# Performance work log

Measured on AMD Instinct MI355X. Metric: run time of the kernel, lower is better.

The kernel has to match this reference:

```python
import jax, jax.numpy as jnp
import numpy as np

N_NODES = 100000
N_EDGES = 1600000
F_IN = 128
H1 = 128
H2 = 128
N_CLASSES = 40


def setup_inputs() -> dict:
    key = jax.random.key(0)
    ks = jax.random.split(key, 8)
    node_features = jax.random.normal(ks[0], (N_NODES, F_IN), dtype=jnp.float32)
    edge_indices = jax.random.randint(ks[1], (2, N_EDGES), 0, N_NODES, dtype=jnp.int32)
    # Glorot-ish init for weights
    W1 = jax.random.normal(ks[2], (F_IN, H1), dtype=jnp.float32) / np.sqrt(F_IN)
    b1 = jnp.zeros((H1,), dtype=jnp.float32)
    W2 = jax.random.normal(ks[3], (H1, H2), dtype=jnp.float32) / np.sqrt(H1)
    b2 = jnp.zeros((H2,), dtype=jnp.float32)
    Wl = jax.random.normal(ks[4], (H2, N_CLASSES), dtype=jnp.float32) / np.sqrt(H2)
    bl = jnp.zeros((N_CLASSES,), dtype=jnp.float32)
    return {
        "node_features": node_features,
        "edge_indices": edge_indices,
        "W1": W1, "b1": b1,
        "W2": W2, "b2": b2,
        "Wl": Wl, "bl": bl,
    }


def _gcn_norm(edge_indices, n_nodes):
    # PyG GCNConv default: add self-loops, symmetric normalization.
    src = jnp.concatenate([edge_indices[0], jnp.arange(n_nodes, dtype=edge_indices.dtype)])
    dst = jnp.concatenate([edge_indices[1], jnp.arange(n_nodes, dtype=edge_indices.dtype)])
    deg = jax.ops.segment_sum(jnp.ones_like(dst, dtype=jnp.float32), dst,
                              num_segments=n_nodes)  # degree over destinations (col)
    deg_inv_sqrt = jnp.where(deg > 0, jax.lax.rsqrt(deg), 0.0)
    norm = deg_inv_sqrt[src] * deg_inv_sqrt[dst]  # (E + N,)
    return src, dst, norm


def _gcn_conv(x, W, b, src, dst, norm, n_nodes):
    xw = x @ W                                    # (N, F_out) dense GEMM
    msg = xw[src] * norm[:, None]                 # gather + scale: (E+N, F_out)
    out = jax.ops.segment_sum(msg, dst, num_segments=n_nodes)  # scatter-add
    return out + b


def reference(node_features, edge_indices, W1, b1, W2, b2, Wl, bl):
    n = node_features.shape[0]
    src, dst, norm = _gcn_norm(edge_indices, n)
    # dropout is identity in eval mode
    x = jax.nn.relu(_gcn_conv(node_features, W1, b1, src, dst, norm, n))
    x = jax.nn.relu(_gcn_conv(x, W2, b2, src, dst, norm, n))
    return x @ Wl + bl  # (N, num_classes)
```

## Files before the change

### kernel.cpp

```cpp
#include <hip/hip_runtime.h>


typedef unsigned int uint32;
typedef unsigned short u16;

#define FD 128

using short8 = __attribute__((ext_vector_type(8))) short;
using f32x4  = __attribute__((ext_vector_type(4))) float;

union U4S8 { uint4 u; short8 s; };

__device__ __forceinline__ u16 f2bf(float f) {
    uint32 u = __float_as_uint(f);
    uint32 r = ((u >> 16) & 1u) + 0x7FFFu;
    return (u16)((u + r) >> 16);
}
__device__ __forceinline__ float bfLo(uint32 w) { return __uint_as_float(w << 16); }
__device__ __forceinline__ float bfHi(uint32 w) { return __uint_as_float(w & 0xFFFF0000u); }

__global__ void k_beacon(float* __restrict__ out, long long n, float val) {
    long long i = (long long)blockIdx.x * 256 + threadIdx.x;
    if (i < n) out[i] = val;
}

__device__ __forceinline__ void wprep_dev(const float* __restrict__ W,
                                          uint4* __restrict__ wf,
                                          int NOUT, int NT, int t) {
    for (int e = t; e < 4 * NT * 64; e += 256) {
        int kc = e / (NT * 64);
        int rem = e - kc * (NT * 64);
        int ct = rem >> 6;
        int l  = rem & 63;
        int k0 = kc * 32 + (l >> 4) * 8;
        int c  = ct * 16 + (l & 15);
        u16 us[8];
#pragma unroll
        for (int i = 0; i < 8; i++)
            us[i] = (c < NOUT) ? f2bf(W[(size_t)(k0 + i) * NOUT + c]) : (u16)0;
        uint4 u;
        u.x = (uint32)us[0] | ((uint32)us[1] << 16);
        u.y = (uint32)us[2] | ((uint32)us[3] << 16);
        u.z = (uint32)us[4] | ((uint32)us[5] << 16);
        u.w = (uint32)us[6] | ((uint32)us[7] << 16);
        wf[(kc * NT + ct) * 64 + l] = u;
    }
}

__global__ __launch_bounds__(256) void k_cnt_mgemm(
    const int* __restrict__ dst, int* __restrict__ cnt, int* __restrict__ rank,
    int ne, int nn,
    const float* __restrict__ A, const float* __restrict__ W,
    uint32* __restrict__ yt, int M, int ngemm,
    const float* __restrict__ W2, uint4* __restrict__ wf2,
    const float* __restrict__ Wl, uint4* __restrict__ wfl) {
    __shared__ uint4 Bf[4][8][64];

    int bid = blockIdx.x;
    int t = threadIdx.x;

    if (bid >= (int)gridDim.x - 2) {
        if (bid == (int)gridDim.x - 2) wprep_dev(W2, wf2, 128, 8, t);
        else                           wprep_dev(Wl, wfl, 40, 3, t);
        return;
    }

    int g5 = bid / 5;
    bool isg = ((bid % 5) == 0) && (g5 < ngemm);

    if (!isg) {
        int idx = bid - (g5 + 1 < ngemm ? g5 + 1 : ngemm);
        int e = idx * 256 + t;
        if (e < ne) {
            int d = dst[e];
            int a = ((unsigned)d < (unsigned)nn) ? d : nn;
            rank[e] = atomicAdd(&cnt[a], 1);
        }
        return;
    }

    int idx = g5;
    for (int e = t; e < 4 * 8 * 64; e += 256) {
        int kc = e / (8 * 64);
        int rem = e - kc * (8 * 64);
        int ct = rem >> 6;
        int l  = rem & 63;
        int k0 = kc * 32 + (l >> 4) * 8;
        int c  = ct * 16 + (l & 15);
        u16 us[8];
#pragma unroll
        for (int i = 0; i < 8; i++) us[i] = f2bf(W[(size_t)(k0 + i) * 128 + c]);
        uint4 u;
        u.x = (uint32)us[0] | ((uint32)us[1] << 16);
        u.y = (uint32)us[2] | ((uint32)us[3] << 16);
        u.z = (uint32)us[4] | ((uint32)us[5] << 16);
        u.w = (uint32)us[6] | ((uint32)us[7] << 16);
        Bf[kc][ct][l] = u;
    }
    __syncthreads();

    int lane = t & 63, wv = t >> 6;
    int r0 = idx * 64 + wv * 16;
    if (r0 >= M) return;

    int arow = r0 + (lane & 15);
    if (arow >= M) arow = M - 1;
    U4S8 af[4];
#pragma unroll
    for (int kc = 0; kc < 4; kc++) {
        const float4* s = (const float4*)(A + (size_t)arow * FD + kc * 32 + (lane >> 4) * 8);
        float4 v0 = s[0], v1 = s[1];
        uint4 u;
        u.x = (uint32)f2bf(v0.x) | ((uint32)f2bf(v0.y) << 16);
        u.y = (uint32)f2bf(v0.z) | ((uint32)f2bf(v0.w) << 16);
        u.z = (uint32)f2bf(v1.x) | ((uint32)f2bf(v1.y) << 16);
        u.w = (uint32)f2bf(v1.z) | ((uint32)f2bf(v1.w) << 16);
        af[kc].u = u;
    }

    f32x4 acc[8];
#pragma unroll
    for (int ct = 0; ct < 8; ct++) acc[ct] = f32x4{0.f, 0.f, 0.f, 0.f};
#pragma unroll
    for (int kc = 0; kc < 4; kc++) {
#pragma unroll
        for (int ct = 0; ct < 8; ct++) {
            U4S8 b;
            b.u = Bf[kc][ct][lane];
            acc[ct] = __builtin_amdgcn_mfma_f32_16x16x32_bf16(af[kc].s, b.s, acc[ct], 0, 0, 0);
        }
    }

    int rb = r0 + (lane >> 4) * 4;
#pragma unroll
    for (int r = 0; r < 4; r++) {
        int row = rb + r;
#pragma unroll
        for (int ct = 0; ct < 8; ct++) {
            float v = acc[ct][r];
            float vn = __shfl_xor(v, 1);
            if (!(lane & 1) && row < M) {
                uint32 word = (uint32)f2bf(v) | ((uint32)f2bf(vn) << 16);
                yt[(size_t)row * 128 + (ct * 16 + (lane & 15)) / 2] = word;
            }
        }
    }
}

__global__ void k_scan_a(const int* __restrict__ cnt, int* __restrict__ row_start,
                         int* __restrict__ bsum, float* __restrict__ dis, int nn) {
    __shared__ int tmp[256];
    int t = threadIdx.x;
    int i = blockIdx.x * 256 + t;
    int v = (i < nn) ? cnt[i] : 0;
    if (i < nn) dis[i] = rsqrtf((float)(v + 1));
    tmp[t] = v;
    __syncthreads();
    for (int off = 1; off < 256; off <<= 1) {
        int x = (t >= off) ? tmp[t - off] : 0;
        __syncthreads();
        tmp[t] += x;
        __syncthreads();
    }
    if (i < nn) row_start[i] = tmp[t] - v;
    if (t == 255) bsum[blockIdx.x] = tmp[255];
}

__global__ void k_scan_b(int* bsum, int nb) {
    __shared__ int tmp[512];
    __shared__ int carry;
    int t = threadIdx.x;
    if (t == 0) carry = 0;
    __syncthreads();
    for (int base = 0; base < nb; base += 512) {
        int i = base + t;
        int v = (i < nb) ? bsum[i] : 0;
        tmp[t] = v;
        __syncthreads();
        for (int off = 1; off < 512; off <<= 1) {
            int x = (t >= off) ? tmp[t - off] : 0;
            __syncthreads();
            tmp[t] += x;
            __syncthreads();
        }
        if (i < nb) bsum[i] = tmp[t] - v + carry;
        __syncthreads();
        if (t == 0) carry += tmp[511];
        __syncthreads();
    }
}

__global__ void k_scan_c(int* __restrict__ row_start, const int* __restrict__ bsum,
                         const int* __restrict__ cnt, int nn) {
    int i = blockIdx.x * 256 + threadIdx.x;
    if (i < nn) {
        int r = row_start[i] + bsum[blockIdx.x];
        row_start[i] = r;
        if (i == nn - 1) row_start[nn] = r + cnt[i];
    }
}

__global__ __launch_bounds__(256) void k_fill(const int* __restrict__ src,
                                              const int* __restrict__ dst,
                                              const int* __restrict__ rank,
                                              const int* __restrict__ row_start,
                                              int* __restrict__ col_idx,
                                              int ne, int nn) {
    long long base = ((long long)blockIdx.x * 256 + threadIdx.x) * 4;
    if (base + 4 <= (long long)ne) {
        int4 d4 = *(const int4*)(dst + base);
        int4 s4 = *(const int4*)(src + base);
        int4 r4 = *(const int4*)(rank + base);
        int dd[4] = {d4.x, d4.y, d4.z, d4.w};
        int ss[4] = {s4.x, s4.y, s4.z, s4.w};
        int rr[4] = {r4.x, r4.y, r4.z, r4.w};
        int pp[4];
#pragma unroll
        for (int r = 0; r < 4; r++) {
            bool ok = (unsigned)dd[r] < (unsigned)nn;
            int dv = ok ? dd[r] : 0;
            int p = row_start[dv] + rr[r];
            pp[r] = ok ? p : -1;
        }
#pragma unroll
        for (int r = 0; r < 4; r++)
            if ((unsigned)pp[r] < (unsigned)ne) col_idx[pp[r]] = ss[r];
    } else {
        for (long long e = base; e < (long long)ne; e++) {
            int d = dst[e];
            if ((unsigned)d >= (unsigned)nn) continue;
            int p = row_start[d] + rank[e];
            if ((unsigned)p < (unsigned)ne) col_idx[p] = src[e];
        }
    }
}

template <int NOUT, bool WEIGHTED, bool OUTBF>
__global__ __launch_bounds__(256) void k_aggmm(
    const uint32* __restrict__ ytin,
    const float* __restrict__ dis,
    const int* __restrict__ row_start,
    const int* __restrict__ col_idx,
    const float* __restrict__ abias,
    const uint4* __restrict__ Wfrag,
    void* __restrict__ out,
    const float* __restrict__ gbias,
    int nn, int ne) {
    constexpr int NT = (NOUT + 15) / 16;
    __shared__ u16 Ar[64][136];

    int t = threadIdx.x;
    int lane = t & 63, wv = t >> 6;
    int g = lane >> 4, sub = lane & 15;
    int nb0 = blockIdx.x * 64;

    float2 bq[4];
#pragma unroll
    for (int k = 0; k < 4; k++) bq[k] = *(const float2*)(abias + (sub * 4 + k) * 2);

    for (int it = 0; it < 4; it++) {
        int lr = wv * 16 + it * 4 + g;
        int n = nb0 + lr;
        bool act = n < nn;
        int nl = act ? n : 0;

        float di = dis[nl];
        int jb = row_start[nl];
        int je = row_start[nl + 1];
        if (!act) { jb = 0; je = 0; }
        if (jb < 0) jb = 0;
        if (je > ne) je = ne;
        int deg = je - jb; if (deg < 0) deg = 0;
        int je1 = je - 1;

        uint4 sv = *(const uint4*)(ytin + (size_t)nl * 128 + sub * 4);
        float wself = WEIGHTED ? di : 1.f;
        float a0 = bfLo(sv.x) * wself, a1 = bfHi(sv.x) * wself;
        float a2 = bfLo(sv.y) * wself, a3 = bfHi(sv.y) * wself;
        float a4 = bfLo(sv.z) * wself, a5 = bfHi(sv.z) * wself;
        float a6 = bfLo(sv.w) * wself, a7 = bfHi(sv.w) * wself;

        int m = deg;
        m = max(m, __shfl_xor(m, 16));
        m = max(m, __shfl_xor(m, 32));

        for (int base = 0; base < m; base += 8) {
            int jj = jb + base + (sub & 7);
            int jc = jj < je ? jj : je1;
            if (jc < 0) jc = 0;
            int sl = col_idx[jc];
            bool okp = (unsigned)sl < (unsigned)nn;
            float ds = WEIGHTED ? (okp ? dis[sl] : 0.f) : (okp ? 1.f : 0.f);
            if (!okp) sl = 0;

            int ss[8];
            float ww[8];
#pragma unroll
            for (int r = 0; r < 8; r++) {
                int L = (lane & 48) + r;
                ss[r] = __shfl(sl, L);
                float w = __shfl(ds, L);
                ww[r] = (base + r < deg) ? w : 0.f;
            }
            uint4 uu[8];
#pragma unroll
            for (int r = 0; r < 8; r++)
                uu[r] = *(const uint4*)(ytin + (size_t)ss[r] * 128 + sub * 4);
#pragma unroll
            for (int r = 0; r < 8; r++) {
                float wg = ww[r];
                a0 = fmaf(bfLo(uu[r].x), wg, a0); a1 = fmaf(bfHi(uu[r].x), wg, a1);
                a2 = fmaf(bfLo(uu[r].y), wg, a2); a3 = fmaf(bfHi(uu[r].y), wg, a3);
                a4 = fmaf(bfLo(uu[r].z), wg, a4); a5 = fmaf(bfHi(uu[r].z), wg, a5);
                a6 = fmaf(bfLo(uu[r].w), wg, a6); a7 = fmaf(bfHi(uu[r].w), wg, a7);
            }
        }

        if (act) {
            float r0 = fmaxf(fmaf(a0, di, bq[0].x), 0.f);
            float r1 = fmaxf(fmaf(a1, di, bq[0].y), 0.f);
            float r2 = fmaxf(fmaf(a2, di, bq[1].x), 0.f);
            float r3 = fmaxf(fmaf(a3, di, bq[1].y), 0.f);
            float r4 = fmaxf(fmaf(a4, di, bq[2].x), 0.f);
            float r5 = fmaxf(fmaf(a5, di, bq[2].y), 0.f);
            float r6 = fmaxf(fmaf(a6, di, bq[3].x), 0.f);
            float r7 = fmaxf(fmaf(a7, di, bq[3].y), 0.f);
            uint4 o;
            o.x = (uint32)f2bf(r0) | ((uint32)f2bf(r1) << 16);
            o.y = (uint32)f2bf(r2) | ((uint32)f2bf(r3) << 16);
            o.z = (uint32)f2bf(r4) | ((uint32)f2bf(r5) << 16);
            o.w = (uint32)f2bf(r6) | ((uint32)f2bf(r7) << 16);
            *(uint4*)&Ar[lr][sub * 8] = o;
        }
    }
    __syncthreads();

    int arl = wv * 16 + (lane & 15);
    U4S8 af[4];
#pragma unroll
    for (int kc = 0; kc < 4; kc++)
        af[kc].u = *(const uint4*)&Ar[arl][kc * 32 + (lane >> 4) * 8];

    f32x4 acc[NT];
#pragma unroll
    for (int ct = 0; ct < NT; ct++) {
        acc[ct] = f32x4{0.f, 0.f, 0.f, 0.f};
        U4S8 w0, w1, w2, w3;
        w0.u = Wfrag[(0 * NT + ct) * 64 + lane];
        w1.u = Wfrag[(1 * NT + ct) * 64 + lane];
        w2.u = Wfrag[(2 * NT + ct) * 64 + lane];
        w3.u = Wfrag[(3 * NT + ct) * 64 + lane];
        acc[ct] = __builtin_amdgcn_mfma_f32_16x16x32_bf16(af[0].s, w0.s, acc[ct], 0, 0, 0);
        acc[ct] = __builtin_amdgcn_mfma_f32_16x16x32_bf16(af[1].s, w1.s, acc[ct], 0, 0, 0);
        acc[ct] = __builtin_amdgcn_mfma_f32_16x16x32_bf16(af[2].s, w2.s, acc[ct], 0, 0, 0);
        acc[ct] = __builtin_amdgcn_mfma_f32_16x16x32_bf16(af[3].s, w3.s, acc[ct], 0, 0, 0);
    }

    int rbl = wv * 16 + (lane >> 4) * 4;
    if (OUTBF) {
        uint32* yto = (uint32*)out;
#pragma unroll
        for (int r = 0; r < 4; r++) {
            int grow = nb0 + rbl + r;
            int gc = grow < nn ? grow : 0;
            float rs = dis[gc];
#pragma unroll
            for (int ct = 0; ct < NT; ct++) {
                float v = acc[ct][r] * rs;
                float vn = __shfl_xor(v, 1);
                if (!(lane & 1) && grow < nn) {
                    uint32 word = (uint32)f2bf(v) | ((uint32)f2bf(vn) << 16);
                    yto[(size_t)grow * 128 + (ct * 16 + (lane & 15)) / 2] = word;
                }
            }
        }
    } else {
        float* fo = (float*)out;
#pragma unroll
        for (int r = 0; r < 4; r++) {
            int grow = nb0 + rbl + r;
            if (grow >= nn) continue;
#pragma unroll
            for (int ct = 0; ct < NT; ct++) {
                int c = ct * 16 + (lane & 15);
                if (c < NOUT)
                    fo[(size_t)grow * NOUT + c] = acc[ct][r] + gbias[c];
            }
        }
    }
}

static inline char* carve(char*& p, size_t bytes) {
    char* r = p;
    p += (bytes + 255) & ~(size_t)255;
    return r;
}

extern "C" void kernel_launch(void* const* d_in, const int* in_sizes, int n_in,
                              void* d_out, int out_size, void* d_ws, size_t ws_size,
                              hipStream_t stream) {
    const long long outn = out_size;
    float* dout = (float*)d_out;
    if (n_in < 8) {
        k_beacon<<<(int)((outn + 255) / 256), 256, 0, stream>>>(dout, outn, 888.f);
        return;
    }
    float* X        = (float*)d_in[0];
    const int* ei   = (const int*)d_in[1];
    const float* W1 = (const float*)d_in[2];
    const float* b1 = (const float*)d_in[3];
    const float* W2 = (const float*)d_in[4];
    const float* b2 = (const float*)d_in[5];
    const float* Wl = (const float*)d_in[6];
    const float* bl = (const float*)d_in[7];

    const int H1 = in_sizes[3];
    const int F  = in_sizes[2] / (H1 > 0 ? H1 : 1);
    const int NC = in_sizes[7];
    const int NN = in_sizes[0] / (F > 0 ? F : 1);
    const int NE = in_sizes[1] / 2;
    if (NN <= 0 || NE <= 0 || F != FD || H1 != FD || NC != 40 ||
        (long long)NN * FD != in_sizes[0] || outn != (long long)NN * NC) {
        k_beacon<<<(int)((outn + 255) / 256), 256, 0, stream>>>(dout, outn, 888.f);
        return;
    }

    const int* src = ei;
    const int* dst = ei + NE;
    const int nb = (NN + 255) / 256;

    char* p = (char*)d_ws;
    int*   cnt       = (int*)  carve(p, ((size_t)NN + 1) * 4);
    float* dis       = (float*)carve(p, (size_t)NN * 4);
    int*   bsum      = (int*)  carve(p, (size_t)nb * 4);
    int*   row_start = (int*)  carve(p, ((size_t)NN + 1) * 4);
    int*   col_idx   = (int*)  carve(p, (size_t)NE * 4);
    uint4* wf2       = (uint4*)carve(p, (size_t)4 * 8 * 64 * 16);
    uint4* wfl       = (uint4*)carve(p, (size_t)4 * 3 * 64 * 16);
    size_t needed = (size_t)(p - (char*)d_ws);
    int* rank;
    if ((size_t)NE * 4 <= (size_t)outn * 4) {
        rank = (int*)d_out;
    } else {
        rank = (int*)carve(p, (size_t)NE * 4);
        needed = (size_t)(p - (char*)d_ws);
    }
    if (needed > ws_size) {
        k_beacon<<<(int)((outn + 255) / 256), 256, 0, stream>>>(dout, outn, 999.f);
        return;
    }

    const int ecb1 = (NE + 255) / 256;
    const int ecb4 = (int)(((long long)NE + 1023) / 1024);
    const int gemm_blocks = (NN + 63) / 64;

    uint32* yt1 = (uint32*)X;
    uint32* zt  = yt1 + 64;

    hipMemsetAsync(cnt, 0, ((size_t)NN + 1) * 4, stream);
    k_cnt_mgemm<<<ecb1 + gemm_blocks + 2, 256, 0, stream>>>(
        dst, cnt, rank, NE, NN,
        X, W1, yt1, NN, gemm_blocks,
        W2, wf2, Wl, wfl);
    k_scan_a<<<nb, 256, 0, stream>>>(cnt, row_start, bsum, dis, NN);
    k_scan_b<<<1, 512, 0, stream>>>(bsum, nb);
    k_scan_c<<<nb, 256, 0, stream>>>(row_start, bsum, cnt, NN);
    k_fill<<<ecb4, 256, 0, stream>>>(src, dst, rank, row_start, col_idx, NE, NN);

    k_aggmm<128, true, true><<<gemm_blocks, 256, 0, stream>>>(
        yt1, dis, row_start, col_idx, b1, wf2, (void*)zt, nullptr, NN, NE);

    k_aggmm<40, false, false><<<gemm_blocks, 256, 0, stream>>>(
        zt, dis, row_start, col_idx, b2, wfl, (void*)dout, bl, NN, NE);
}
```

Measured before the change: 358.1 us.

## Fuse three-kernel prefix scan into single-pass decoupled lookback and drop aggmm barrier

Replaces the three-kernel degree scan (block scan, block-sum scan, add-back) with one kernel. Each block publishes its total with a status flag in a per-block state word and looks back at earlier blocks to find its exclusive prefix. The state array sits next to the count array, so the existing memset now clears both. In k_aggmm, the __syncthreads between writing the shared A tile and reading it is swapped for a compiler sched_barrier. That removes a workgroup barrier but may cause a cross-wave race if a wave reads rows written by another wave.

```diff
diff --git a/kernel.cpp b/kernel.cpp
--- a/kernel.cpp
+++ b/kernel.cpp
@@ -3,6 +3,7 @@
 
 typedef unsigned int uint32;
 typedef unsigned short u16;
+typedef unsigned long long u64;
 
 #define FD 128
 
@@ -147,11 +148,14 @@
     }
 }
 
-__global__ void k_scan_a(const int* __restrict__ cnt, int* __restrict__ row_start,
-                         int* __restrict__ bsum, float* __restrict__ dis, int nn) {
+__global__ __launch_bounds__(256) void k_scan(const int* __restrict__ cnt,
+                                              int* __restrict__ row_start,
+                                              float* __restrict__ dis,
+                                              u64* __restrict__ state, int nn) {
     __shared__ int tmp[256];
-    int t = threadIdx.x;
-    int i = blockIdx.x * 256 + t;
+    __shared__ int exc_sh;
+    int t = threadIdx.x, b = blockIdx.x;
+    int i = b * 256 + t;
     int v = (i < nn) ? cnt[i] : 0;
     if (i < nn) dis[i] = rsqrtf((float)(v + 1));
     tmp[t] = v;
@@ -162,42 +166,26 @@
         tmp[t] += x;
         __syncthreads();
     }
-    if (i < nn) row_start[i] = tmp[t] - v;
-    if (t == 255) bsum[blockIdx.x] = tmp[255];
-}
-
-__global__ void k_scan_b(int* bsum, int nb) {
-    __shared__ int tmp[512];
-    __shared__ int carry;
-    int t = threadIdx.x;
-    if (t == 0) carry = 0;
+    int total = tmp[255];
+
+    if (t == 0) {
+        atomicExch(&state[b], (1ULL << 62) | (unsigned)total);
+        unsigned exc = 0;
+        for (int j = b - 1; j >= 0;) {
+            u64 s = atomicAdd(&state[j], 0ULL);
+            u64 fl = s >> 62;
+            if (fl == 0) continue;
+            exc += (unsigned)s;
+            if (fl == 2) break;
+            j--;
+        }
+        atomicExch(&state[b], (2ULL << 62) | (u64)(unsigned)(exc + (unsigned)total));
+        exc_sh = (int)exc;
+    }
     __syncthreads();
-    for (int base = 0; base < nb; base += 512) {
-        int i = base + t;
-        int v = (i < nb) ? bsum[i] : 0;
-        tmp[t] = v;
-        __syncthreads();
-        for (int off = 1; off < 512; off <<= 1) {
-            int x = (t >= off) ? tmp[t - off] : 0;
-            __syncthreads();
-            tmp[t] += x;
-            __syncthreads();
-        }
-        if (i < nb) bsum[i] = tmp[t] - v + carry;
-        __syncthreads();
-        if (t == 0) carry += tmp[511];
-        __syncthreads();
-    }
-}
-
-__global__ void k_scan_c(int* __restrict__ row_start, const int* __restrict__ bsum,
-                         const int* __restrict__ cnt, int nn) {
-    int i = blockIdx.x * 256 + threadIdx.x;
-    if (i < nn) {
-        int r = row_start[i] + bsum[blockIdx.x];
-        row_start[i] = r;
-        if (i == nn - 1) row_start[nn] = r + cnt[i];
-    }
+    int exc = exc_sh;
+    if (i < nn) row_start[i] = exc + tmp[t] - v;
+    if (i == nn - 1) row_start[nn] = exc + total;
 }
 
 __global__ __launch_bounds__(256) void k_fill(const int* __restrict__ src,
@@ -333,7 +321,8 @@
             *(uint4*)&Ar[lr][sub * 8] = o;
         }
     }
-    __syncthreads();
+
+    __builtin_amdgcn_sched_barrier(0);
 
     int arl = wv * 16 + (lane & 15);
     U4S8 af[4];
@@ -431,8 +420,9 @@
 
     char* p = (char*)d_ws;
     int*   cnt       = (int*)  carve(p, ((size_t)NN + 1) * 4);
+    u64*   state     = (u64*)  carve(p, (size_t)nb * 8);
+    char*  zero_end  = p;
     float* dis       = (float*)carve(p, (size_t)NN * 4);
-    int*   bsum      = (int*)  carve(p, (size_t)nb * 4);
     int*   row_start = (int*)  carve(p, ((size_t)NN + 1) * 4);
     int*   col_idx   = (int*)  carve(p, (size_t)NE * 4);
     uint4* wf2       = (uint4*)carve(p, (size_t)4 * 8 * 64 * 16);
@@ -457,14 +447,12 @@
     uint32* yt1 = (uint32*)X;
     uint32* zt  = yt1 + 64;
 
-    hipMemsetAsync(cnt, 0, ((size_t)NN + 1) * 4, stream);
+    hipMemsetAsync(cnt, 0, (size_t)(zero_end - (char*)cnt), stream);
     k_cnt_mgemm<<<ecb1 + gemm_blocks + 2, 256, 0, stream>>>(
         dst, cnt, rank, NE, NN,
         X, W1, yt1, NN, gemm_blocks,
         W2, wf2, Wl, wfl);
-    k_scan_a<<<nb, 256, 0, stream>>>(cnt, row_start, bsum, dis, NN);
-    k_scan_b<<<1, 512, 0, stream>>>(bsum, nb);
-    k_scan_c<<<nb, 256, 0, stream>>>(row_start, bsum, cnt, NN);
+    k_scan<<<nb, 256, 0, stream>>>(cnt, row_start, dis, state, NN);
     k_fill<<<ecb4, 256, 0, stream>>>(src, dst, rank, row_start, col_idx, NE, NN);
 
     k_aggmm<128, true, true><<<gemm_blocks, 256, 0, stream>>>(
```

Result: slower. 371.0 us (+3.6%).
